# Performance work log

Measured on AMD Instinct MI355X. Metric: run time of the kernel, lower is better.

Reference implementation:

```python
import jax, jax.numpy as jnp
import numpy as np

B, T, D, H = 2, 2048, 1024, 16
HD = D // H  # head_dim = 64


def setup_inputs() -> dict:
    key = jax.random.key(0)
    ks = jax.random.split(key, 6)
    x = jax.random.normal(ks[0], (B, T, D), dtype=jnp.float32)
    wq = jax.random.normal(ks[1], (D, D), dtype=jnp.float32) * (D ** -0.5)
    wk = jax.random.normal(ks[2], (D, D), dtype=jnp.float32) * (D ** -0.5)
    wv = jax.random.normal(ks[3], (D, D), dtype=jnp.float32) * (D ** -0.5)
    wo = jax.random.normal(ks[4], (D, D), dtype=jnp.float32) * (D ** -0.5)
    # RoPE tables: standard inverse-frequency angles, shape [T, head_dim]
    inv_freq = 1.0 / (10000.0 ** (jnp.arange(0, HD, 2, dtype=jnp.float32) / HD))
    ang = jnp.arange(T, dtype=jnp.float32)[:, None] * inv_freq[None, :]  # [T, HD/2]
    ang = jnp.concatenate([ang, ang], axis=-1)  # [T, HD]
    cos, sin = jnp.cos(ang), jnp.sin(ang)
    # causal mask [1,1,T,T]: True where attention is allowed
    mask = jnp.tril(jnp.ones((T, T), dtype=bool))[None, None]
    return {"x": x, "wq": wq, "wk": wk, "wv": wv, "wo": wo,
            "cos": cos, "sin": sin, "mask": mask}


def rotate_half(u):
    u1, u2 = jnp.split(u, 2, axis=-1)
    return jnp.concatenate([-u2, u1], axis=-1)


def reference(x, wq, wk, wv, wo, cos, sin, mask):
    b, t, c = x.shape
    # projections (nn.Linear: y = x @ W^T), reshape to [B, H, T, HD]
    def proj(w):
        return (x @ w.T).reshape(b, t, H, HD).transpose(0, 2, 1, 3)
    q, k, v = proj(wq), proj(wk), proj(wv)
    # inline RoPE: cos/sin broadcast [1,1,T,HD]
    co = cos[:t][None, None]
    si = sin[:t][None, None]
    q = q * co + rotate_half(q) * si
    k = k * co + rotate_half(k) * si
    # scaled dot-product attention with causal mask
    att = jnp.einsum("bhqd,bhkd->bhqk", q, k) * (HD ** -0.5)
    att = jnp.where(mask[:, :, :t, :t], att, -jnp.inf)
    att = jax.nn.softmax(att, axis=-1)
    out = jnp.einsum("bhqk,bhkd->bhqd", att, v)
    out = out.transpose(0, 2, 1, 3).reshape(b, t, c)
    return out @ wo.T
```

## Files before the change

kernel.cpp:

```cpp
#include <hip/hip_runtime.h>
#include <hip/hip_bf16.h>
#include <type_traits>

#define B_  2
#define T_  2048
#define D_  1024
#define H_  16
#define HD_ 64

typedef __attribute__((ext_vector_type(8))) short bf16x8;
typedef __attribute__((ext_vector_type(4))) float f32x4;

__device__ __forceinline__ unsigned short f2b(float x) {
  union { __hip_bfloat16 h; unsigned short u; } c;
  c.h = __float2bfloat16(x);
  return c.u;
}

__device__ __forceinline__ void ld_g2l_16(const unsigned short* g, unsigned short* l) {
  auto gp = (const __attribute__((address_space(1))) unsigned int*)g;
  auto lp = (__attribute__((address_space(3))) unsigned int*)l;
  __builtin_amdgcn_global_load_lds(gp, lp, 16, 0, 0);
}

__device__ __forceinline__ void cast_job(int blk, const float* __restrict__ x,
                                         const float* __restrict__ wq, const float* __restrict__ wk,
                                         const float* __restrict__ wv, const float* __restrict__ wo,
                                         unsigned short* __restrict__ xb,
                                         unsigned short* __restrict__ wp) {
  const float* src;
  unsigned short* dst;
  size_t off;
  if (blk < 2048) {
    src = x; dst = xb; off = (size_t)blk * 2048;
  } else {
    int t = (blk - 2048) >> 9;
    int r = (blk - 2048) & 511;
    src = (t == 0) ? wq : (t == 1) ? wk : (t == 2) ? wv : wo;
    dst = wp + (size_t)t * 1048576;
    off = (size_t)r * 2048;
  }
  size_t i = off + threadIdx.x * 8;
  float4 a = *(const float4*)(src + i);
  float4 b = *(const float4*)(src + i + 4);
  unsigned short h[8] = {f2b(a.x), f2b(a.y), f2b(a.z), f2b(a.w),
                         f2b(b.x), f2b(b.y), f2b(b.z), f2b(b.w)};
  *(uint4*)(dst + i) = *(uint4*)h;
}

template <typename OutT, int MROWS>
__device__ __forceinline__ void gemm_core(unsigned short* __restrict__ shm,
                                          const unsigned short* __restrict__ A,
                                          const unsigned short* __restrict__ Bw,
                                          OutT* __restrict__ C, int K, int Ldc,
                                          int rope_mode, const float* __restrict__ cosT,
                                          const float* __restrict__ sinT, int tok0) {
  constexpr int MT = MROWS / 32;
  constexpr int ASZ = MROWS * 32;
  const int tid = threadIdx.x;
  const int lane = tid & 63;
  const int w = tid >> 6;
  const int m16 = lane & 15;
  const int quad = lane >> 4;
  const int wm = w >> 1, wn = w & 1;
  const int rl = lane >> 2;
  const int cl = (lane & 3) * 8;

  f32x4 acc[MT][4];
#pragma unroll
  for (int i = 0; i < MT; i++)
#pragma unroll
    for (int j = 0; j < 4; j++) acc[i][j] = (f32x4){0.f, 0.f, 0.f, 0.f};

  auto stage = [&](int it, int bs) {
    int k0 = it * 32;
#pragma unroll
    for (int t = 0; t < MROWS / 64; t++) {
      int seg = w * 16 + t * 64;
      ld_g2l_16(A + (size_t)(seg + rl) * K + k0 + cl, shm + bs * ASZ + seg * 32);
    }
#pragma unroll
    for (int j2 = 0; j2 < 2; j2++) {
      int seg = w * 32 + j2 * 16;
      ld_g2l_16(Bw + (size_t)(seg + rl) * K + k0 + cl, shm + 2 * ASZ + bs * 4096 + seg * 32);
    }
  };

  const int nit = K / 32;
  stage(0, 0);
  __syncthreads();
  for (int it = 0; it < nit; it++) {
    int cur = it & 1;
    if (it + 1 < nit) stage(it + 1, cur ^ 1);
    bf16x8 af[MT], bfr[4];
#pragma unroll
    for (int mt = 0; mt < MT; mt++)
      af[mt] = *(const bf16x8*)(shm + cur * ASZ + (wm * (MT * 16) + mt * 16 + m16) * 32 + quad * 8);
#pragma unroll
    for (int nt = 0; nt < 4; nt++)
      bfr[nt] = *(const bf16x8*)(shm + 2 * ASZ + cur * 4096 + (wn * 64 + nt * 16 + m16) * 32 + quad * 8);
#pragma unroll
    for (int mt = 0; mt < MT; mt++)
#pragma unroll
      for (int nt = 0; nt < 4; nt++)
        acc[mt][nt] = __builtin_amdgcn_mfma_f32_16x16x32_bf16(af[mt], bfr[nt], acc[mt][nt], 0, 0, 0);
    __syncthreads();
  }

  if (rope_mode == 3) {
    if constexpr (std::is_same_v<OutT, unsigned short> && MROWS == 128) {
#pragma unroll
      for (int mt = 0; mt < MT; mt++)
#pragma unroll
        for (int nt = 0; nt < 4; nt++) {
          int lc = wn * 64 + nt * 16 + m16;
          int s  = wm * 16 + mt * 4 + quad;
          int ph = s ^ (lc & 31);
          unsigned short pk[4] = {f2b(acc[mt][nt][0]), f2b(acc[mt][nt][1]),
                                  f2b(acc[mt][nt][2]), f2b(acc[mt][nt][3])};
          *(uint2*)&shm[lc * 128 + ph * 4] = *(uint2*)pk;
        }
      __syncthreads();
#pragma unroll
      for (int i = 0; i < 16; i++) {
        int li = i * 256 + tid;
        int r = li >> 5, c2 = li & 31;
        int ph = c2 ^ (r & 31);
        *(uint2*)(C + (size_t)r * T_ + c2 * 4) = *(const uint2*)&shm[r * 128 + ph * 4];
      }
    }
    return;
  }

  if (rope_mode == 1 || rope_mode == 2) {
    float scale = (rope_mode == 2) ? 0.18033688011112042f : 1.f;
#pragma unroll
    for (int mt = 0; mt < MT; mt++)
#pragma unroll
      for (int reg = 0; reg < 4; reg++) {
        int t = (tok0 + wm * (MT * 16) + mt * 16 + quad * 4 + reg) & (T_ - 1);
#pragma unroll
        for (int nt = 0; nt < 2; nt++) {
          int d = nt * 16 + m16;
          float co = cosT[t * HD_ + d] * scale;
          float si = sinT[t * HD_ + d] * scale;
          float lo = acc[mt][nt][reg], hi = acc[mt][nt + 2][reg];
          acc[mt][nt][reg]     = lo * co - hi * si;
          acc[mt][nt + 2][reg] = hi * co + lo * si;
        }
      }
  }
#pragma unroll
  for (int mt = 0; mt < MT; mt++)
#pragma unroll
    for (int nt = 0; nt < 4; nt++)
#pragma unroll
      for (int reg = 0; reg < 4; reg++) {
        OutT* p = C + (size_t)(wm * (MT * 16) + mt * 16 + quad * 4 + reg) * Ldc + wn * 64 + nt * 16 + m16;
        if constexpr (std::is_same_v<OutT, float>) *p = acc[mt][nt][reg];
        else *p = f2b(acc[mt][nt][reg]);
      }
}

__device__ __forceinline__ void qkv_job(unsigned short* shm, int nb, int bm,
                                        const unsigned short* __restrict__ xb,
                                        const unsigned short* __restrict__ wp,
                                        unsigned short* __restrict__ qkv,
                                        const float* __restrict__ cosT,
                                        const float* __restrict__ sinT) {
  const int mi = nb >> 3;
  const int bn = (nb & 7) * 128;
  if (mi == 2) {
    unsigned short* Cv = qkv + 2 * (4096ull * D_) +
                         (size_t)(bm >> 11) * (size_t)(H_ * HD_) * T_ +
                         (size_t)bn * T_ + (bm & (T_ - 1));
    gemm_core<unsigned short, 128>(shm, xb + (size_t)bm * D_,
                                   wp + (size_t)(2 * 1024 + bn) * D_,
                                   Cv, D_, T_, 3, nullptr, nullptr, bm);
  } else {
    const int rope_mode = (mi == 0) ? 2 : 1;
    gemm_core<unsigned short, 128>(shm, xb + (size_t)bm * D_,
                                   wp + (size_t)(mi * 1024 + bn) * D_,
                                   qkv + (size_t)mi * (4096ull * D_) + (size_t)bm * D_ + bn,
                                   D_, D_, rope_mode, cosT, sinT, bm);
  }
}

__device__ __forceinline__ void attn_job(unsigned short* pool, int x,
                                         const unsigned short* __restrict__ Q,
                                         const unsigned short* __restrict__ K,
                                         const unsigned short* __restrict__ VT,
                                         unsigned short* __restrict__ O) {
  unsigned short* qp = pool;
  unsigned short* ks = pool + 4608;
  unsigned short* vs = pool + 4608 + 8192;

  const int tid = threadIdx.x;
  const int lane = tid & 63;
  const int w = tid >> 6;
  const int m16 = lane & 15;
  const int quad = lane >> 4;
  const int swz = m16 & 7;
  const int pc0 = quad ^ swz;
  const int pc1 = pc0 ^ 4;

  const int qt = 31 - (x >> 5);
  const int bh = x & 31;
  const int b = bh >> 4, h = bh & 15;
  const int q0 = qt * 64;

  const unsigned short* Qb = Q + ((size_t)b * T_ + q0) * D_ + h * HD_;
  const unsigned short* Kb = K + (size_t)b * T_ * D_ + h * HD_;
  const unsigned short* VTb = VT + ((size_t)b * H_ + h) * HD_ * T_;

#pragma unroll
  for (int i = 0; i < 2; i++) {
    int idx = tid + i * 256;
    int r = idx >> 3, c = idx & 7;
    *(bf16x8*)&qp[r * 72 + c * 8] = *(const bf16x8*)(Qb + (size_t)r * D_ + c * 8);
  }

  auto stage_kv = [&](int kt, int bs) {
    int rs = lane >> 3;
    int cs = ((lane & 7) ^ rs) * 8;
    int gr = w * 16 + rs;
    ld_g2l_16(Kb + (size_t)(kt * 64 + gr) * D_ + cs,      ks + bs * 4096 + (w * 16) * 64);
    ld_g2l_16(Kb + (size_t)(kt * 64 + gr + 8) * D_ + cs,  ks + bs * 4096 + (w * 16 + 8) * 64);
    ld_g2l_16(VTb + (size_t)gr * T_ + kt * 64 + cs,       vs + bs * 4096 + (w * 16) * 64);
    ld_g2l_16(VTb + (size_t)(gr + 8) * T_ + kt * 64 + cs, vs + bs * 4096 + (w * 16 + 8) * 64);
  };

  f32x4 o_acc[4];
#pragma unroll
  for (int dt = 0; dt < 4; dt++) o_acc[dt] = (f32x4){0.f, 0.f, 0.f, 0.f};
  float m_i = -1e30f, l_i = 0.f;
  const int rg = q0 + w * 16 + m16;

  stage_kv(0, 0);
  __syncthreads();
  bf16x8 q_frag[2];
  q_frag[0] = *(const bf16x8*)&qp[(w * 16 + m16) * 72 + quad * 8];
  q_frag[1] = *(const bf16x8*)&qp[(w * 16 + m16) * 72 + 32 + quad * 8];

  for (int t = 0; t <= qt; t++) {
    int cur = t & 1;
    if (t < qt) stage_kv(t + 1, cur ^ 1);

    const unsigned short* kc = ks + cur * 4096;
    const unsigned short* vc = vs + cur * 4096;
    f32x4 sf[4];
    __builtin_amdgcn_s_setprio(1);
#pragma unroll
    for (int jt = 0; jt < 4; jt++) {
      bf16x8 a0 = *(const bf16x8*)&kc[(jt * 16 + m16) * 64 + pc0 * 8];
      bf16x8 a1 = *(const bf16x8*)&kc[(jt * 16 + m16) * 64 + pc1 * 8];
      f32x4 acc = (f32x4){0.f, 0.f, 0.f, 0.f};
      acc = __builtin_amdgcn_mfma_f32_16x16x32_bf16(a0, q_frag[0], acc, 0, 0, 0);
      acc = __builtin_amdgcn_mfma_f32_16x16x32_bf16(a1, q_frag[1], acc, 0, 0, 0);
      sf[jt] = acc;
    }
    __builtin_amdgcn_s_setprio(0);
    if (t == qt) {
#pragma unroll
      for (int jt = 0; jt < 4; jt++)
#pragma unroll
        for (int reg = 0; reg < 4; reg++) {
          int jg = t * 64 + jt * 16 + quad * 4 + reg;
          if (jg > rg) sf[jt][reg] = -1e30f;
        }
    }
    float mx = sf[0][0];
#pragma unroll
    for (int jt = 0; jt < 4; jt++)
#pragma unroll
      for (int reg = 0; reg < 4; reg++) mx = fmaxf(mx, sf[jt][reg]);
    mx = fmaxf(mx, __shfl_xor(mx, 16, 64));
    mx = fmaxf(mx, __shfl_xor(mx, 32, 64));
    if (!__all(mx <= m_i + 8.f)) {
      float mn = fmaxf(m_i, mx);
      float alpha = exp2f(m_i - mn);
      l_i *= alpha;
#pragma unroll
      for (int dt = 0; dt < 4; dt++)
#pragma unroll
        for (int reg = 0; reg < 4; reg++) o_acc[dt][reg] *= alpha;
      m_i = mn;
    }
    float lt = 0.f;
    float p[4][4];
#pragma unroll
    for (int jt = 0; jt < 4; jt++)
#pragma unroll
      for (int reg = 0; reg < 4; reg++) {
        p[jt][reg] = exp2f(sf[jt][reg] - m_i);
        lt += p[jt][reg];
      }
#pragma unroll
    for (int jt = 0; jt < 4; jt++) {
      unsigned short pk[4] = {f2b(p[jt][0]), f2b(p[jt][1]), f2b(p[jt][2]), f2b(p[jt][3])};
      *(uint2*)&qp[(w * 16 + m16) * 72 + jt * 16 + quad * 4] = *(uint2*)pk;
    }
    bf16x8 bp0 = *(const bf16x8*)&qp[(w * 16 + m16) * 72 + quad * 8];
    bf16x8 bp1 = *(const bf16x8*)&qp[(w * 16 + m16) * 72 + 32 + quad * 8];
    __builtin_amdgcn_s_setprio(1);
#pragma unroll
    for (int dt = 0; dt < 4; dt++) {
      int rowd = dt * 16 + m16;
      bf16x8 a0 = *(const bf16x8*)&vc[rowd * 64 + pc0 * 8];
      bf16x8 a1 = *(const bf16x8*)&vc[rowd * 64 + pc1 * 8];
      o_acc[dt] = __builtin_amdgcn_mfma_f32_16x16x32_bf16(a0, bp0, o_acc[dt], 0, 0, 0);
      o_acc[dt] = __builtin_amdgcn_mfma_f32_16x16x32_bf16(a1, bp1, o_acc[dt], 0, 0, 0);
    }
    __builtin_amdgcn_s_setprio(0);
    lt += __shfl_xor(lt, 16, 64);
    lt += __shfl_xor(lt, 32, 64);
    l_i += lt;
    __syncthreads();
  }

  float inv = 1.f / l_i;
#pragma unroll
  for (int dt = 0; dt < 4; dt++) {
    unsigned short ok[4];
#pragma unroll
    for (int reg = 0; reg < 4; reg++) ok[reg] = f2b(o_acc[dt][reg] * inv);
    *(uint2*)&qp[(w * 16 + m16) * 72 + dt * 16 + quad * 4] = *(uint2*)ok;
  }
  __syncthreads();
  unsigned short* Ob = O + ((size_t)b * T_ + q0) * D_ + h * HD_;
#pragma unroll
  for (int i = 0; i < 2; i++) {
    int idx = tid + i * 256;
    int r = idx >> 3, c = idx & 7;
    *(bf16x8*)(Ob + (size_t)r * D_ + c * 8) = *(const bf16x8*)&qp[r * 72 + c * 8];
  }
}

__global__ void __launch_bounds__(256)
cast_all(const float* __restrict__ x, const float* __restrict__ wq,
         const float* __restrict__ wk, const float* __restrict__ wv,
         const float* __restrict__ wo, unsigned short* __restrict__ xb,
         unsigned short* __restrict__ wp) {
  cast_job(blockIdx.x, x, wq, wk, wv, wo, xb, wp);
}

__global__ void __launch_bounds__(256)
gemm_qkv(const unsigned short* __restrict__ xb, const unsigned short* __restrict__ wp,
         unsigned short* __restrict__ qkv, const float* __restrict__ cosT,
         const float* __restrict__ sinT) {
  __shared__ __align__(16) unsigned short shm[16384];
  qkv_job(shm, blockIdx.x, blockIdx.y * 128, xb, wp, qkv, cosT, sinT);
}

__global__ void __launch_bounds__(256)
gemm_out(const unsigned short* __restrict__ Ab, const unsigned short* __restrict__ wob,
         float* __restrict__ C) {
  __shared__ __align__(16) unsigned short shm[12288];
  const int bn = blockIdx.x * 128;
  const int bm = blockIdx.y * 64;
  gemm_core<float, 64>(shm, Ab + (size_t)bm * D_, wob + (size_t)bn * D_,
                       C + (size_t)bm * D_ + bn, D_, D_, 0, nullptr, nullptr, 0);
}

__global__ void __launch_bounds__(256, 3)
attn_kernel(const unsigned short* __restrict__ Q, const unsigned short* __restrict__ K,
            const unsigned short* __restrict__ VT, unsigned short* __restrict__ O) {
  __shared__ __align__(16) unsigned short pool[20992];
  attn_job(pool, blockIdx.x, Q, K, VT, O);
}

extern "C" void kernel_launch(void* const* d_in, const int* in_sizes, int n_in,
                              void* d_out, int out_size, void* d_ws, size_t ws_size,
                              hipStream_t stream) {
  const float* x    = (const float*)d_in[0];
  const float* wq   = (const float*)d_in[1];
  const float* wk   = (const float*)d_in[2];
  const float* wv   = (const float*)d_in[3];
  const float* wo   = (const float*)d_in[4];
  const float* cosT = (const float*)d_in[5];
  const float* sinT = (const float*)d_in[6];
  float* out = (float*)d_out;

  const size_t NTOK = (size_t)B_ * T_;
  const size_t SZ   = NTOK * D_;
  unsigned short* xb   = (unsigned short*)d_ws;
  unsigned short* Wp   = xb + SZ;
  unsigned short* QKVh = Wp + 4 * 1048576;
  unsigned short* Ab   = QKVh + 3 * SZ;

  cast_all<<<4096, 256, 0, stream>>>(x, wq, wk, wv, wo, xb, Wp);
  gemm_qkv<<<dim3(24, 32), 256, 0, stream>>>(xb, Wp, QKVh, cosT, sinT);
  attn_kernel<<<1024, 256, 0, stream>>>(QKVh, QKVh + SZ, QKVh + 2 * SZ, Ab);
  gemm_out<<<dim3(8, 64), 256, 0, stream>>>(Ab, Wp + 3 * 1048576, out);
}
```

Before: 204.5 us.

## Swizzle attention Q/P LDS tile, compute row sums via MFMA, raise occupancy

The Q/P staging buffer in the attention kernel drops its padded 72-element row stride for a 64-element stride with an XOR swizzle. This shrinks LDS use per block so launch bounds can ask for four blocks per CU instead of three. The per-tile softmax row sum is now computed with two MFMAs against a vector of bf16 ones, replacing the scalar adds and cross-lane shuffles. This sums the bf16-rounded probabilities, which changes numerics slightly, and the tighter register budget for four blocks may cause spills.

New measurement: 204.2 us. No clear change (-0.2%).

```diff
diff --git a/kernel.cpp b/kernel.cpp
--- a/kernel.cpp
+++ b/kernel.cpp
@@ -192,8 +192,8 @@
                                          const unsigned short* __restrict__ VT,
                                          unsigned short* __restrict__ O) {
   unsigned short* qp = pool;
-  unsigned short* ks = pool + 4608;
-  unsigned short* vs = pool + 4608 + 8192;
+  unsigned short* ks = pool + 4096;
+  unsigned short* vs = pool + 4096 + 8192;
 
   const int tid = threadIdx.x;
   const int lane = tid & 63;
@@ -217,7 +217,7 @@
   for (int i = 0; i < 2; i++) {
     int idx = tid + i * 256;
     int r = idx >> 3, c = idx & 7;
-    *(bf16x8*)&qp[r * 72 + c * 8] = *(const bf16x8*)(Qb + (size_t)r * D_ + c * 8);
+    *(bf16x8*)&qp[r * 64 + ((c ^ (r & 7)) * 8)] = *(const bf16x8*)(Qb + (size_t)r * D_ + c * 8);
   }
 
   auto stage_kv = [&](int kt, int bs) {
@@ -234,13 +234,18 @@
 #pragma unroll
   for (int dt = 0; dt < 4; dt++) o_acc[dt] = (f32x4){0.f, 0.f, 0.f, 0.f};
   float m_i = -1e30f, l_i = 0.f;
-  const int rg = q0 + w * 16 + m16;
+  const int row = w * 16 + m16;
+  const int rs7 = row & 7;
+  const int rg = q0 + row;
+
+  const short one_bf = (short)0x3F80;
+  bf16x8 ones = {one_bf, one_bf, one_bf, one_bf, one_bf, one_bf, one_bf, one_bf};
 
   stage_kv(0, 0);
   __syncthreads();
   bf16x8 q_frag[2];
-  q_frag[0] = *(const bf16x8*)&qp[(w * 16 + m16) * 72 + quad * 8];
-  q_frag[1] = *(const bf16x8*)&qp[(w * 16 + m16) * 72 + 32 + quad * 8];
+  q_frag[0] = *(const bf16x8*)&qp[row * 64 + ((quad ^ rs7) * 8)];
+  q_frag[1] = *(const bf16x8*)&qp[row * 64 + (((4 + quad) ^ rs7) * 8)];
 
   for (int t = 0; t <= qt; t++) {
     int cur = t & 1;
@@ -286,22 +291,23 @@
         for (int reg = 0; reg < 4; reg++) o_acc[dt][reg] *= alpha;
       m_i = mn;
     }
-    float lt = 0.f;
     float p[4][4];
 #pragma unroll
     for (int jt = 0; jt < 4; jt++)
 #pragma unroll
-      for (int reg = 0; reg < 4; reg++) {
+      for (int reg = 0; reg < 4; reg++)
         p[jt][reg] = exp2f(sf[jt][reg] - m_i);
-        lt += p[jt][reg];
-      }
 #pragma unroll
     for (int jt = 0; jt < 4; jt++) {
       unsigned short pk[4] = {f2b(p[jt][0]), f2b(p[jt][1]), f2b(p[jt][2]), f2b(p[jt][3])};
-      *(uint2*)&qp[(w * 16 + m16) * 72 + jt * 16 + quad * 4] = *(uint2*)pk;
-    }
-    bf16x8 bp0 = *(const bf16x8*)&qp[(w * 16 + m16) * 72 + quad * 8];
-    bf16x8 bp1 = *(const bf16x8*)&qp[(w * 16 + m16) * 72 + 32 + quad * 8];
+      int cL = jt * 2 + (quad >> 1);
+      *(uint2*)&qp[row * 64 + ((cL ^ rs7) * 8) + (quad & 1) * 4] = *(uint2*)pk;
+    }
+    bf16x8 bp0 = *(const bf16x8*)&qp[row * 64 + ((quad ^ rs7) * 8)];
+    bf16x8 bp1 = *(const bf16x8*)&qp[row * 64 + (((4 + quad) ^ rs7) * 8)];
+    f32x4 lacc = (f32x4){0.f, 0.f, 0.f, 0.f};
+    lacc = __builtin_amdgcn_mfma_f32_16x16x32_bf16(ones, bp0, lacc, 0, 0, 0);
+    lacc = __builtin_amdgcn_mfma_f32_16x16x32_bf16(ones, bp1, lacc, 0, 0, 0);
     __builtin_amdgcn_s_setprio(1);
 #pragma unroll
     for (int dt = 0; dt < 4; dt++) {
@@ -312,9 +318,7 @@
       o_acc[dt] = __builtin_amdgcn_mfma_f32_16x16x32_bf16(a1, bp1, o_acc[dt], 0, 0, 0);
     }
     __builtin_amdgcn_s_setprio(0);
-    lt += __shfl_xor(lt, 16, 64);
-    lt += __shfl_xor(lt, 32, 64);
-    l_i += lt;
+    l_i += lacc[0];
     __syncthreads();
   }
 
@@ -324,7 +328,8 @@
     unsigned short ok[4];
 #pragma unroll
     for (int reg = 0; reg < 4; reg++) ok[reg] = f2b(o_acc[dt][reg] * inv);
-    *(uint2*)&qp[(w * 16 + m16) * 72 + dt * 16 + quad * 4] = *(uint2*)ok;
+    int cL = dt * 2 + (quad >> 1);
+    *(uint2*)&qp[row * 64 + ((cL ^ rs7) * 8) + (quad & 1) * 4] = *(uint2*)ok;
   }
   __syncthreads();
   unsigned short* Ob = O + ((size_t)b * T_ + q0) * D_ + h * HD_;
@@ -332,7 +337,7 @@
   for (int i = 0; i < 2; i++) {
     int idx = tid + i * 256;
     int r = idx >> 3, c = idx & 7;
-    *(bf16x8*)(Ob + (size_t)r * D_ + c * 8) = *(const bf16x8*)&qp[r * 72 + c * 8];
+    *(bf16x8*)(Ob + (size_t)r * D_ + c * 8) = *(const bf16x8*)&qp[r * 64 + ((c ^ (r & 7)) * 8)];
   }
 }
 
@@ -362,10 +367,10 @@
                        C + (size_t)bm * D_ + bn, D_, D_, 0, nullptr, nullptr, 0);
 }
 
-__global__ void __launch_bounds__(256, 3)
+__global__ void __launch_bounds__(256, 4)
 attn_kernel(const unsigned short* __restrict__ Q, const unsigned short* __restrict__ K,
             const unsigned short* __restrict__ VT, unsigned short* __restrict__ O) {
-  __shared__ __align__(16) unsigned short pool[20992];
+  __shared__ __align__(16) unsigned short pool[20480];
   attn_job(pool, blockIdx.x, Q, K, VT, O);
 }
 
```
